# Optimization experiments

Hardware: AMD Instinct MI355X
Metric: run time of the kernel (lower is better)

The kernel has to match this reference:

```python
import jax, jax.numpy as jnp
import numpy as np

C = 32          # middle_channels
N_DOWN = 13     # layers 2..14, stride 2
DENSITY = 0.01  # nnz fraction of the 2048x2048 sparse matrix


def _conv(x, w):
    # centered SAME conv; inactive sites hold zeros so they contribute nothing,
    # matching MinkowskiConvolution's sum over existing neighbor coordinates.
    return jax.lax.conv_general_dilated(
        x, w, window_strides=(1, 1), padding='SAME',
        dimension_numbers=('NHWC', 'HWIO', 'NHWC'))


def _downsample_mask(mask):
    # ME stride-2 output coords = stride-quantized input coords -> OR over 2x2 block
    return jax.lax.reduce_window(mask, 0.0, jax.lax.max, (1, 2, 2), (1, 2, 2), 'SAME')


def _layer(x, mask, w, stride):
    y = _conv(x, w)
    if stride > 1:
        y = y[:, ::stride, ::stride, :]   # value at quantized coordinate u
        mask = _downsample_mask(mask)
    y = jax.nn.relu(y) * mask[..., None]  # ReLU on active sites, keep inactive = 0
    return y, mask


def _global_avg_pool(x, mask):
    cnt = jnp.maximum(jnp.sum(mask, axis=(1, 2)), 1.0)  # number of active coords
    return jnp.sum(x, axis=(1, 2)) / cnt[:, None]       # [B, C]


def setup_inputs() -> dict:
    key = jax.random.key(0)
    ks = jax.random.split(key, 8)
    H = W = 2048
    mask = (jax.random.uniform(ks[0], (1, H, W)) < DENSITY).astype(jnp.float32)
    x = jax.random.normal(ks[1], (1, H, W, 1), dtype=jnp.float32) * mask[..., None]
    # kaiming_normal fan_out (nonlinearity='relu') for conv kernels, bias=False in ME
    w1 = jax.random.normal(ks[2], (5, 5, 1, C), dtype=jnp.float32) * np.float32((2.0 / (5 * 5 * C)) ** 0.5)
    ws = jax.random.normal(ks[3], (N_DOWN, 3, 3, C, C), dtype=jnp.float32) * np.float32((2.0 / (3 * 3 * C)) ** 0.5)
    wm1 = jax.random.normal(ks[4], (C * 14, 256), dtype=jnp.float32) * np.float32((1.0 / (C * 14)) ** 0.5)
    bm1 = jnp.zeros((256,), jnp.float32)
    wm2 = jax.random.normal(ks[5], (256, 128), dtype=jnp.float32) * np.float32((1.0 / 256) ** 0.5)
    bm2 = jnp.zeros((128,), jnp.float32)
    return {'x': x, 'mask': mask, 'w1': w1, 'ws': ws,
            'wm1': wm1, 'bm1': bm1, 'wm2': wm2, 'bm2': bm2}


def reference(x, mask, w1, ws, wm1, bm1, wm2, bm2):
    y, m = _layer(x, mask, w1, stride=1)          # layer1: k=5, s=1
    pools = [_global_avg_pool(y, m)]
    for i in range(N_DOWN):                       # layers 2..14: k=3, s=2
        y, m = _layer(y, m, ws[i], stride=2)
        pools.append(_global_avg_pool(y, m))
    feat = jnp.concatenate(pools, axis=-1)        # [B, 32*14]
    h = jax.nn.relu(feat @ wm1 + bm1)
    return h @ wm2 + bm2                          # [B, 128]
```

## Files before the change

kernel.cpp:

```cpp
#include <hip/hip_runtime.h>

#define NLVL 14
#define NSHARD 16

struct ZeroArgs { unsigned long long zoff[13]; };

struct TailArgs {
    char* ws;
    const float* wm1; const float* bm1;
    const float* wm2; const float* bm2;
    float* out;
    unsigned long long idx8, idx9, idx10;
    unsigned long long nbr8, nbr9, nbr10;
    unsigned long long val7, val8, val9;
    int cap8, cap9, cap10;
};

__device__ __forceinline__ float fma4(float4 v, float4 w, float acc) {
    acc = fmaf(v.x, w.x, acc);
    acc = fmaf(v.y, w.y, acc);
    acc = fmaf(v.z, w.z, acc);
    return fmaf(v.w, w.w, acc);
}

__device__ __forceinline__ int cnt_load(const int* p) {
    return __hip_atomic_load(p, __ATOMIC_RELAXED, __HIP_MEMORY_SCOPE_AGENT);
}

__device__ __forceinline__ int block_scan_base(int mycnt, int* gcnt, int& myoff) {
    __shared__ int wsum[4];
    __shared__ int base;
    __syncthreads();
    int lane = threadIdx.x & 63, wid = threadIdx.x >> 6;
    int scan = mycnt;
    #pragma unroll
    for (int d = 1; d < 64; d <<= 1) {
        int tv = __shfl_up(scan, d, 64);
        if (lane >= d) scan += tv;
    }
    if (lane == 63) wsum[wid] = scan;
    __syncthreads();
    if (threadIdx.x == 0) {
        int tot = 0;
        #pragma unroll
        for (int i = 0; i < 4; i++) { int tv = wsum[i]; wsum[i] = tot; tot += tv; }
        base = tot ? atomicAdd(gcnt, tot) : 0;
    }
    __syncthreads();
    myoff = wsum[wid] + scan - mycnt;
    return base;
}

__device__ void compact0_tile(const float4* __restrict__ mask4, int* __restrict__ idxmap,
                              int* __restrict__ coords, int* __restrict__ cnt, int cap, int tile) {
    int t = threadIdx.x;
    int g0 = tile * 1024 + t;
    float4 m[4];
    #pragma unroll
    for (int j = 0; j < 4; j++) m[j] = mask4[g0 + j * 256];
    int pr[16];
    int mycnt = 0;
    #pragma unroll
    for (int j = 0; j < 4; j++) {
        pr[4 * j + 0] = m[j].x > 0.5f;
        pr[4 * j + 1] = m[j].y > 0.5f;
        pr[4 * j + 2] = m[j].z > 0.5f;
        pr[4 * j + 3] = m[j].w > 0.5f;
        mycnt += pr[4 * j] + pr[4 * j + 1] + pr[4 * j + 2] + pr[4 * j + 3];
    }
    int myoff;
    int base = block_scan_base(mycnt, cnt, myoff);
    int slot = base + myoff;
    #pragma unroll
    for (int j = 0; j < 4; j++) {
        int e0 = (g0 + j * 256) << 2;
        int wv[4];
        #pragma unroll
        for (int k = 0; k < 4; k++) {
            wv[k] = -1;
            if (pr[4 * j + k]) {
                int sl = slot++;
                if (sl < cap) { wv[k] = sl; coords[sl] = e0 + k; }
            }
        }
        *(int4*)(idxmap + e0) = make_int4(wv[0], wv[1], wv[2], wv[3]);
    }
}

__device__ void down_nbr(const int* __restrict__ idx_in, int HinB,
                         int* __restrict__ idx_out, int* __restrict__ nbr_out,
                         int* __restrict__ cnt_out, int HoutB, int cap_out,
                         int zofs, int bb) {
    int Hout = 1 << HoutB, Hin = 1 << HinB;
    int S = Hout * Hout;
    int S4 = (S + 3) >> 2;
    int o4 = bb * 256 + threadIdx.x;
    int e0 = o4 << 2;
    int jv[4][9];
    int pr[4] = {0, 0, 0, 0};
    #pragma unroll
    for (int k = 0; k < 4; k++)
        #pragma unroll
        for (int tap = 0; tap < 9; tap++) jv[k][tap] = -1;
    if (o4 < S4) {
        if (HoutB >= 2) {
            int r = e0 >> HoutB, c0 = e0 & (Hout - 1);
            int w[3][12];
            #pragma unroll
            for (int a = 0; a < 3; a++) {
                int rr = 2 * r + a - 1;
                bool rok = (unsigned)rr < (unsigned)Hin;
                const int* rowp = idx_in + ((size_t)(rok ? rr : 0) << HinB) + 2 * c0;
                int4 L = (rok && c0 > 0) ? *(const int4*)(rowp - 4) : make_int4(-1, -1, -1, -1);
                int4 M = rok ? *(const int4*)rowp : make_int4(-1, -1, -1, -1);
                int4 R = rok ? *(const int4*)(rowp + 4) : make_int4(-1, -1, -1, -1);
                w[a][0] = L.x; w[a][1] = L.y; w[a][2]  = L.z; w[a][3]  = L.w;
                w[a][4] = M.x; w[a][5] = M.y; w[a][6]  = M.z; w[a][7]  = M.w;
                w[a][8] = R.x; w[a][9] = R.y; w[a][10] = R.z; w[a][11] = R.w;
            }
            #pragma unroll
            for (int k = 0; k < 4; k++) {
                #pragma unroll
                for (int a = 0; a < 3; a++)
                    #pragma unroll
                    for (int b = 0; b < 3; b++)
                        jv[k][a * 3 + b] = w[a][2 * k + b + 3];
                pr[k] = ((jv[k][4] & jv[k][5] & jv[k][7] & jv[k][8]) >= 0);
            }
        } else {
            #pragma unroll
            for (int k = 0; k < 4; k++) {
                int p = e0 + k;
                if (p < S) {
                    int r = p >> HoutB, c = p & (Hout - 1);
                    #pragma unroll
                    for (int a = 0; a < 3; a++)
                        #pragma unroll
                        for (int b = 0; b < 3; b++) {
                            int rr = 2 * r + a - 1, cc = 2 * c + b - 1;
                            if ((unsigned)rr < (unsigned)Hin && (unsigned)cc < (unsigned)Hin)
                                jv[k][a * 3 + b] = idx_in[((size_t)rr << HinB) + cc];
                        }
                    pr[k] = ((jv[k][4] & jv[k][5] & jv[k][7] & jv[k][8]) >= 0);
                }
            }
        }
    }
    int mycnt = pr[0] + pr[1] + pr[2] + pr[3];
    int myoff;
    int base = block_scan_base(mycnt, cnt_out, myoff);
    int slot = base + myoff;
    int wv[4] = {-1, -1, -1, -1};
    #pragma unroll
    for (int k = 0; k < 4; k++) {
        if (pr[k]) {
            int sl = slot++;
            if (sl < cap_out) {
                wv[k] = sl;
                #pragma unroll
                for (int tap = 0; tap < 9; tap++) {
                    int j = jv[k][tap];
                    nbr_out[sl * 9 + tap] = (j < 0) ? zofs : (j << 7);
                }
            }
        }
    }
    if (o4 < S4) {
        if (S >= 4) *(int4*)(idx_out + e0) = make_int4(wv[0], wv[1], wv[2], wv[3]);
        else {
            #pragma unroll
            for (int k = 0; k < 4; k++) if (e0 + k < S) idx_out[e0 + k] = wv[k];
        }
    }
}

__device__ void down_small_wave(const int* __restrict__ idx_in, int HinB,
                                int* __restrict__ idx_out, int* __restrict__ nbr_out,
                                int* __restrict__ cnt_out, int HoutB, int cap_out,
                                int zofs) {
    int t = threadIdx.x;
    int Hout = 1 << HoutB, Hin = 1 << HinB, S = Hout * Hout;
    int p = t;
    int jv[9];
    int pr = 0;
    #pragma unroll
    for (int tap = 0; tap < 9; tap++) jv[tap] = -1;
    if (p < S) {
        int r = p >> HoutB, c = p & (Hout - 1);
        #pragma unroll
        for (int a = 0; a < 3; a++)
            #pragma unroll
            for (int b = 0; b < 3; b++) {
                int rr = 2 * r + a - 1, cc = 2 * c + b - 1;
                if ((unsigned)rr < (unsigned)Hin && (unsigned)cc < (unsigned)Hin)
                    jv[a * 3 + b] = idx_in[(rr << HinB) + cc];
            }
        pr = ((jv[4] & jv[5] & jv[7] & jv[8]) >= 0);
    }
    int scan = pr;
    #pragma unroll
    for (int d = 1; d < 64; d <<= 1) {
        int tv = __shfl_up(scan, d, 64);
        if (t >= d) scan += tv;
    }
    int myoff = scan - pr;
    int tot = __shfl(scan, 63, 64);
    if (p < S) {
        int wv = -1;
        if (pr && myoff < cap_out) {
            wv = myoff;
            #pragma unroll
            for (int tap = 0; tap < 9; tap++) {
                int j = jv[tap];
                nbr_out[myoff * 9 + tap] = (j < 0) ? zofs : (j << 7);
            }
        }
        idx_out[p] = wv;
    }
    if (t == 0 && tot) atomicAdd(cnt_out, tot);
}

__device__ void conv_small_1024(const char* __restrict__ vprevb,
                                const float* __restrict__ wlvl,
                                const int* __restrict__ nbr, int n,
                                float* __restrict__ vals, float* __restrict__ poolp) {
    __shared__ __align__(16) float s_in[576 * 32];
    int t = threadIdx.x;
    int ciq = t & 7, co = (t >> 3) & 31, sp = t >> 8;
    float4 wreg[9];
    #pragma unroll
    for (int tap = 0; tap < 9; tap++)
        wreg[tap] = *(const float4*)(wlvl + ((tap * 32 + co) << 5) + (ciq << 2));
    int items = n * 72;
    for (int i = t; i < items; i += 1024) {
        int row = i >> 3, q = i & 7;
        int jb = nbr[row];
        *(float4*)&s_in[(row << 5) + (q << 2)] =
            *(const float4*)(vprevb + jb + (q << 4));
    }
    __syncthreads();
    float ps = 0.f;
    #pragma unroll 1
    for (int gp = 0; gp < 16; gp++) {
        int g = gp * 4 + sp;
        if (g >= n) break;
        float a0 = 0.f;
        #pragma unroll
        for (int tap = 0; tap < 9; tap++) {
            float4 v = *(const float4*)&s_in[((g * 9 + tap) << 5) + (ciq << 2)];
            a0 = fma4(v, wreg[tap], a0);
        }
        a0 += __shfl_xor(a0, 1); a0 += __shfl_xor(a0, 2); a0 += __shfl_xor(a0, 4);
        if (ciq == 0) {
            float r0 = fmaxf(a0, 0.f);
            vals[((size_t)g << 5) + co] = r0;
            ps += r0;
        }
    }
    if (ciq == 0 && ps != 0.f) atomicAdd(&poolp[co], ps);
}

__device__ void conv_bs(const char* __restrict__ vprevb, const float* __restrict__ wlvl,
                        const int* __restrict__ nbr, int n,
                        float* __restrict__ vals, float* __restrict__ poolp,
                        int b0, int nbk, int shard) {
    __shared__ int s_j[144];
    __shared__ __align__(16) float s_in[144 * 32];
    int t = threadIdx.x;
    int ciq = t & 7, coh = (t >> 3) & 15, sp = t >> 7;
    float4 wreg[9][2];
    #pragma unroll
    for (int tap = 0; tap < 9; tap++) {
        wreg[tap][0] = *(const float4*)(wlvl + ((tap * 32 + coh) << 5) + (ciq << 2));
        wreg[tap][1] = *(const float4*)(wlvl + ((tap * 32 + coh + 16) << 5) + (ciq << 2));
    }
    float ps0 = 0.f, ps1 = 0.f;
    int ngr = (n + 15) >> 4;
    for (int grp = b0; grp < ngr; grp += nbk) {
        __syncthreads();
        if (t < 144) {
            int gi = grp * 144 + t;
            s_j[t] = (gi < n * 9) ? nbr[gi] : 0;
        }
        __syncthreads();
        #pragma unroll
        for (int i = t; i < 1152; i += 256) {
            int row = i >> 3, q = i & 7;
            *(float4*)&s_in[(row << 5) + (q << 2)] =
                *(const float4*)(vprevb + s_j[row] + (q << 4));
        }
        __syncthreads();
        #pragma unroll
        for (int gp = 0; gp < 8; gp++) {
            int g = gp * 2 + sp;
            int s = (grp << 4) + g;
            float4 v[9];
            #pragma unroll
            for (int tap = 0; tap < 9; tap++)
                v[tap] = *(const float4*)&s_in[((g * 9 + tap) << 5) + (ciq << 2)];
            float a0 = 0.f, a1 = 0.f;
            #pragma unroll
            for (int tap = 0; tap < 9; tap++) {
                a0 = fma4(v[tap], wreg[tap][0], a0);
                a1 = fma4(v[tap], wreg[tap][1], a1);
            }
            a0 += __shfl_xor(a0, 1); a0 += __shfl_xor(a0, 2); a0 += __shfl_xor(a0, 4);
            a1 += __shfl_xor(a1, 1); a1 += __shfl_xor(a1, 2); a1 += __shfl_xor(a1, 4);
            if (ciq == 0 && s < n) {
                float r0 = fmaxf(a0, 0.f), r1 = fmaxf(a1, 0.f);
                vals[((size_t)s << 5) + coh] = r0;
                vals[((size_t)s << 5) + coh + 16] = r1;
                ps0 += r0; ps1 += r1;
            }
        }
    }
    if (ciq == 0 && (ps0 != 0.f || ps1 != 0.f)) {
        atomicAdd(&poolp[shard * 448 + coh], ps0);
        atomicAdd(&poolp[shard * 448 + coh + 16], ps1);
    }
}

__device__ void conv0_bs(const float* __restrict__ x, const float* __restrict__ w1,
                         const int* __restrict__ coords0, int n,
                         float* __restrict__ vals0, float* __restrict__ poolp,
                         int b0, int nbk, int shard) {
    __shared__ float lw[800];
    __shared__ float lx[8][28];
    __shared__ float red[256];
    int t = threadIdx.x;
    for (int i = t; i < 800; i += 256) lw[i] = w1[i];
    int sl = t >> 5, ch = t & 31;
    float psum = 0.f;
    int ngr = (n + 7) >> 3;
    for (int grp = b0; grp < ngr; grp += nbk) {
        __syncthreads();
        if (t < 200) {
            int slot = t / 25, tap = t - slot * 25;
            int s = (grp << 3) + slot;
            float v = 0.f;
            if (s < n) {
                int p = coords0[s];
                int r = p >> 11, c = p & 2047;
                int a = tap / 5, b = tap - a * 5;
                int rr = r + a - 2, cc = c + b - 2;
                if ((unsigned)rr < 2048u && (unsigned)cc < 2048u)
                    v = x[(rr << 11) + cc];
            }
            lx[slot][tap] = v;
        }
        __syncthreads();
        int s = (grp << 3) + sl;
        float acc = 0.f;
        #pragma unroll
        for (int tap = 0; tap < 25; tap++)
            acc = fmaf(lx[sl][tap], lw[tap * 32 + ch], acc);
        if (s < n) {
            float r0 = fmaxf(acc, 0.f);
            vals0[((size_t)s << 5) + ch] = r0;
            psum += r0;
        }
    }
    __syncthreads();
    red[t] = psum;
    __syncthreads();
    if (t < 32) {
        float tot = 0.f;
        #pragma unroll
        for (int q = 0; q < 8; q++) tot += red[t + 32 * q];
        if (tot != 0.f) atomicAdd(&poolp[shard * 448 + t], tot);
    }
}

__global__ __launch_bounds__(256) void k_f0(
    const float4* __restrict__ mask4, int* __restrict__ idxmap,
    int* __restrict__ coords, int* __restrict__ cnt, int cap,
    const float* __restrict__ w, float* __restrict__ wt,
    char* __restrict__ wsbase, ZeroArgs za) {
    if (blockIdx.x == 1492) {
        for (int i = threadIdx.x; i < 13 * 32; i += 256)
            *(float*)(wsbase + za.zoff[i >> 5] + ((i & 31) << 2)) = 0.f;
        return;
    }
    if (blockIdx.x >= 1024) {
        int t = (int)(blockIdx.x - 1024) * 256 + threadIdx.x;
        if (t < 13 * 9 * 32 * 32) {
            int ci = t & 31, co = (t >> 5) & 31, tp = t >> 10;
            wt[(tp << 10) + (co << 5) + ci] = w[(tp << 10) + (ci << 5) + co];
        }
        return;
    }
    compact0_tile(mask4, idxmap, coords, cnt, cap, blockIdx.x);
}

__global__ __launch_bounds__(256) void k_f1(
    const int* __restrict__ idx0, int* __restrict__ idx1, int* __restrict__ nbr1,
    int* __restrict__ cnt1, int cap1, int zofs1,
    const float* __restrict__ x, const float* __restrict__ w1,
    const int* __restrict__ coords0, const int* __restrict__ cnt0, int cap0,
    float* __restrict__ vals0, float* __restrict__ poolp,
    const float* __restrict__ wm1, const float* __restrict__ wm2, float* __restrict__ dummy) {
    if (blockIdx.x < 1024) {
        down_nbr(idx0, 11, idx1, nbr1, cnt1, 10, cap1, zofs1, blockIdx.x);
        return;
    }
    if (blockIdx.x >= 5120) {
        int t = (int)(blockIdx.x - 5120) * 256 + threadIdx.x;
        const float4* a = (const float4*)wm1;
        const float4* b = (const float4*)wm2;
        float acc = 0.f;
        for (int i = t; i < 28672; i += 6144) { float4 v = a[i]; acc += v.x + v.y + v.z + v.w; }
        for (int i = t; i < 8192; i += 6144)  { float4 v = b[i]; acc += v.x + v.y + v.z + v.w; }
        if (acc == 1234.56789f) dummy[0] = acc;
        return;
    }
    int n = *cnt0; if (n > cap0) n = cap0;
    conv0_bs(x, w1, coords0, n, vals0, poolp, blockIdx.x - 1024, 4096, blockIdx.x & (NSHARD - 1));
}

__global__ __launch_bounds__(256) void k_flevel(
    int downB,
    const int* __restrict__ idx_in, int HinB,
    int* __restrict__ idx_out, int* __restrict__ nbr_out, int* __restrict__ cnt_out,
    int HoutB, int cap_out, int zofs,
    const char* __restrict__ vprevb, const float* __restrict__ wlvl,
    const int* __restrict__ nbr_c, const int* __restrict__ cnt_c, int cap_c,
    float* __restrict__ vals_c, float* __restrict__ poolp) {
    if ((int)blockIdx.x < downB) {
        down_nbr(idx_in, HinB, idx_out, nbr_out, cnt_out, HoutB, cap_out, zofs, blockIdx.x);
        return;
    }
    int n = *cnt_c; if (n > cap_c) n = cap_c;
    conv_bs(vprevb, wlvl, nbr_c, n, vals_c, poolp,
            blockIdx.x - downB, gridDim.x - downB, blockIdx.x & (NSHARD - 1));
}

__global__ __launch_bounds__(1024) void k_tail3(TailArgs a) {
    char* ws = a.ws;
    int* cnt = (int*)ws;
    float* poolsh = (float*)(ws + 256);
    float* wt = (float*)(ws + 32768);
    int t = threadIdx.x;

    if (t < 64)
        down_small_wave((const int*)(ws + a.idx8), 3, (int*)(ws + a.idx9),
                        (int*)(ws + a.nbr9), cnt + 9, 2, a.cap9, a.cap8 * 128);
    __syncthreads();
    {
        int n8 = cnt_load(cnt + 8); if (n8 > a.cap8) n8 = a.cap8;
        conv_small_1024((const char*)(ws + a.val7), wt + (size_t)7 * 9216,
                        (const int*)(ws + a.nbr8), n8,
                        (float*)(ws + a.val8), poolsh + 8 * 32);
    }
    __syncthreads();
    if (t < 64)
        down_small_wave((const int*)(ws + a.idx9), 2, (int*)(ws + a.idx10),
                        (int*)(ws + a.nbr10), cnt + 10, 1, a.cap10, a.cap9 * 128);
    __syncthreads();
    {
        int n9 = cnt_load(cnt + 9); if (n9 > a.cap9) n9 = a.cap9;
        conv_small_1024((const char*)(ws + a.val8), wt + (size_t)8 * 9216,
                        (const int*)(ws + a.nbr9), n9,
                        (float*)(ws + a.val9), poolsh + 9 * 32);
    }
    __syncthreads();

    const char* vals9b = (const char*)(ws + a.val9);
    const int* nbr10 = (const int*)(ws + a.nbr10);
    const int* idx10 = (const int*)(ws + a.idx10);
    __shared__ __align__(16) float v10[128];
    __shared__ float v11[32], v12[32], v13[32];
    __shared__ float feat[448], h[256], part[1024];
    __shared__ int s_i10[4], s_n10;
    int ciq = t & 7, co = (t >> 3) & 31, s = t >> 8;
    int ciq16 = ciq << 4;
    if (t == 0) s_n10 = cnt_load(cnt + 10);
    if (t < 4) s_i10[t] = idx10[t];
    __syncthreads();
    int n10 = s_n10; if (n10 > 4) n10 = 4;
    {
        const float* wl = wt + (size_t)9 * 9216;
        float4 wreg[9];
        #pragma unroll
        for (int tap = 0; tap < 9; tap++)
            wreg[tap] = *(const float4*)(wl + ((tap * 32 + co) << 5) + (ciq << 2));
        bool live = s < n10;
        int sb = live ? s : 0;
        float a0 = 0.f;
        #pragma unroll
        for (int tap = 0; tap < 9; tap++)
            a0 = fma4(*(const float4*)(vals9b + nbr10[sb * 9 + tap] + ciq16), wreg[tap], a0);
        a0 += __shfl_xor(a0, 1); a0 += __shfl_xor(a0, 2); a0 += __shfl_xor(a0, 4);
        if (ciq == 0 && live) v10[s * 32 + co] = fmaxf(a0, 0.f);
    }
    __syncthreads();
    int i10[4] = {s_i10[0], s_i10[1], s_i10[2], s_i10[3]};
    int nbr11[9];
    #pragma unroll
    for (int tap = 0; tap < 9; tap++) {
        int aa = tap / 3, bb = tap - aa * 3;
        int rr = aa - 1, cc = bb - 1;
        nbr11[tap] = ((unsigned)rr < 2u && (unsigned)cc < 2u) ? i10[rr * 2 + cc] : -1;
    }
    int n11 = ((nbr11[4] & nbr11[5] & nbr11[7] & nbr11[8]) >= 0) ? 1 : 0;
    if (s == 0) {
        const float* wl = wt + (size_t)10 * 9216;
        float a0 = 0.f;
        #pragma unroll
        for (int tap = 0; tap < 9; tap++) {
            int j = nbr11[tap];
            if (j >= 0) {
                float4 wv = *(const float4*)(wl + ((tap * 32 + co) << 5) + (ciq << 2));
                a0 = fma4(*(const float4*)(&v10[(j << 5) + (ciq << 2)]), wv, a0);
            }
        }
        a0 += __shfl_xor(a0, 1); a0 += __shfl_xor(a0, 2); a0 += __shfl_xor(a0, 4);
        if (ciq == 0) v11[co] = n11 ? fmaxf(a0, 0.f) : 0.f;
    }
    __syncthreads();
    if (s == 0) {
        const float* wl = wt + (size_t)11 * 9216;
        float4 wv = *(const float4*)(wl + ((4 * 32 + co) << 5) + (ciq << 2));
        float a0 = n11 ? fma4(*(const float4*)(&v11[ciq << 2]), wv, 0.f) : 0.f;
        a0 += __shfl_xor(a0, 1); a0 += __shfl_xor(a0, 2); a0 += __shfl_xor(a0, 4);
        if (ciq == 0) v12[co] = n11 ? fmaxf(a0, 0.f) : 0.f;
    }
    __syncthreads();
    if (s == 0) {
        const float* wl = wt + (size_t)12 * 9216;
        float4 wv = *(const float4*)(wl + ((4 * 32 + co) << 5) + (ciq << 2));
        float a0 = n11 ? fma4(*(const float4*)(&v12[ciq << 2]), wv, 0.f) : 0.f;
        a0 += __shfl_xor(a0, 1); a0 += __shfl_xor(a0, 2); a0 += __shfl_xor(a0, 4);
        if (ciq == 0) v13[co] = n11 ? fmaxf(a0, 0.f) : 0.f;
    }
    __syncthreads();
    if (t < 320) {
        float sum = 0.f;
        #pragma unroll
        for (int sh = 0; sh < NSHARD; sh++) sum += poolsh[sh * 448 + t];
        float c = (float)cnt_load(cnt + (t >> 5)); if (c < 1.f) c = 1.f;
        feat[t] = sum / c;
    }
    if (t < 32) {
        float s10 = 0.f;
        for (int q = 0; q < n10; q++) s10 += v10[q * 32 + t];
        float c10 = (float)n10; if (c10 < 1.f) c10 = 1.f;
        feat[320 + t] = s10 / c10;
        feat[352 + t] = n11 ? v11[t] : 0.f;
        feat[384 + t] = n11 ? v12[t] : 0.f;
        feat[416 + t] = n11 ? v13[t] : 0.f;
    }
    __syncthreads();
    {
        int j = t & 255, chunk = t >> 8;
        float acc = (chunk == 0) ? a.bm1[j] : 0.f;
        int k0 = chunk * 112;
        #pragma unroll 8
        for (int k = k0; k < k0 + 112; k++) acc = fmaf(feat[k], a.wm1[k * 256 + j], acc);
        part[t] = acc;
    }
    __syncthreads();
    if (t < 256)
        h[t] = fmaxf(part[t] + part[t + 256] + part[t + 512] + part[t + 768], 0.f);
    __syncthreads();
    {
        int j2 = t & 127, c2 = t >> 7;
        float a2 = (c2 == 0) ? a.bm2[j2] : 0.f;
        int kk0 = c2 * 32;
        #pragma unroll 8
        for (int k = kk0; k < kk0 + 32; k++) a2 = fmaf(h[k], a.wm2[k * 128 + j2], a2);
        part[t] = a2;
    }
    __syncthreads();
    if (t < 128) {
        float sum = 0.f;
        #pragma unroll
        for (int c = 0; c < 8; c++) sum += part[t + 128 * c];
        a.out[t] = sum;
    }
}

extern "C" void kernel_launch(void* const* d_in, const int* in_sizes, int n_in,
                              void* d_out, int out_size, void* d_ws, size_t ws_size,
                              hipStream_t stream) {
    const float* x    = (const float*)d_in[0];
    const float* mask = (const float*)d_in[1];
    const float* w1   = (const float*)d_in[2];
    const float* wsrc = (const float*)d_in[3];
    const float* wm1  = (const float*)d_in[4];
    const float* bm1  = (const float*)d_in[5];
    const float* wm2  = (const float*)d_in[6];
    const float* bm2  = (const float*)d_in[7];
    float* out = (float*)d_out;
    char* ws = (char*)d_ws;

    static const int Hb[NLVL]   = {11, 10, 9, 8, 7, 6, 5, 4, 3, 2, 1, 0, 0, 0};
    static const int caps[NLVL] = {45056, 43008, 43008, 34816, 16384, 4096,
                                   1024, 256, 64, 16, 4, 1, 1, 1};

    size_t pool_off = 256;
    size_t wt_off = 32768;
    size_t off = wt_off + (size_t)13 * 9 * 1024 * 4;
    off = (off + 255) & ~(size_t)255;
    size_t coord0_off = off; off += (size_t)caps[0] * 4; off = (off + 255) & ~(size_t)255;
    size_t idx_off[NLVL], nbr_off[NLVL], val_off[NLVL];
    for (int l = 0; l < NLVL; l++) {
        size_t S = (size_t)(1 << Hb[l]) * (1 << Hb[l]);
        size_t sb = S * 4; if (sb < 16) sb = 16;
        idx_off[l] = off; off += sb; off = (off + 255) & ~(size_t)255;
        if (l >= 1) { nbr_off[l] = off; off += (size_t)caps[l] * 36; off = (off + 255) & ~(size_t)255; }
        else nbr_off[l] = 0;
        val_off[l] = off; off += (size_t)(caps[l] + 1) * 128; off = (off + 255) & ~(size_t)255;
    }

    int* cnt = (int*)ws;
    float* poolsh = (float*)(ws + pool_off);
    float* dummy = (float*)(ws + 128);
    float* wt = (float*)(ws + wt_off);

    ZeroArgs za;
    for (int l = 0; l < 13; l++) za.zoff[l] = val_off[l] + (size_t)caps[l] * 128;

    hipMemsetAsync(ws, 0, 32768, stream);

    k_f0<<<1493, 256, 0, stream>>>(
        (const float4*)mask, (int*)(ws + idx_off[0]), (int*)(ws + coord0_off),
        cnt, caps[0], wsrc, wt, ws, za);

    k_f1<<<5144, 256, 0, stream>>>(
        (const int*)(ws + idx_off[0]), (int*)(ws + idx_off[1]), (int*)(ws + nbr_off[1]),
        cnt + 1, caps[1], caps[0] * 128,
        x, w1, (const int*)(ws + coord0_off), cnt, caps[0],
        (float*)(ws + val_off[0]), poolsh, wm1, wm2, dummy);

    for (int i = 2; i <= 8; i++) {
        int lc = i - 1;
        int Hout = 1 << Hb[i];
        int S4 = (Hout * Hout + 3) >> 2;
        int downB = (S4 + 255) >> 8; if (downB < 1) downB = 1;
        int convB = (caps[lc] + 15) >> 4;
        if (convB > 768) convB = 768;
        k_flevel<<<downB + convB, 256, 0, stream>>>(
            downB,
            (const int*)(ws + idx_off[i - 1]), Hb[i - 1],
            (int*)(ws + idx_off[i]), (int*)(ws + nbr_off[i]), cnt + i, Hb[i], caps[i],
            caps[i - 1] * 128,
            (const char*)(ws + val_off[lc - 1]), wt + (size_t)(lc - 1) * 9216,
            (const int*)(ws + nbr_off[lc]), cnt + lc, caps[lc],
            (float*)(ws + val_off[lc]), poolsh + lc * 32);
    }

    TailArgs ta;
    ta.ws = ws;
    ta.wm1 = wm1; ta.bm1 = bm1; ta.wm2 = wm2; ta.bm2 = bm2;
    ta.out = out;
    ta.idx8 = idx_off[8];  ta.idx9 = idx_off[9];  ta.idx10 = idx_off[10];
    ta.nbr8 = nbr_off[8];  ta.nbr9 = nbr_off[9];  ta.nbr10 = nbr_off[10];
    ta.val7 = val_off[7];  ta.val8 = val_off[8];  ta.val9 = val_off[9];
    ta.cap8 = caps[8]; ta.cap9 = caps[9]; ta.cap10 = caps[10];
    k_tail3<<<1, 1024, 0, stream>>>(ta);
}
```

Before: 257.8 us.

## Double-buffer conv_bs gather with async global-to-LDS loads and index prefetch

The neighbour-feature gather in conv_bs now uses global_load_lds (16-byte direct-to-LDS loads) into a double-buffered shared tile. The next group's tile is issued before the current group is computed, and the neighbour indices for the group after that are preloaded into a register. The goal is to hide gather latency behind the FMA work and drop the register staging of the old load loop. In exchange it doubles LDS use, which may lower occupancy, and it depends on the barrier at the top of the loop to wait for the async LDS writes before they are read.

```diff
diff --git a/kernel.cpp b/kernel.cpp
--- a/kernel.cpp
+++ b/kernel.cpp
@@ -26,6 +26,10 @@
 __device__ __forceinline__ int cnt_load(const int* p) {
     return __hip_atomic_load(p, __ATOMIC_RELAXED, __HIP_MEMORY_SCOPE_AGENT);
 }
+
+#define GLDS16(gsrc, ldst) __builtin_amdgcn_global_load_lds( \
+    (const __attribute__((address_space(1))) void*)(gsrc),   \
+    (__attribute__((address_space(3))) void*)(ldst), 16, 0, 0)
 
 __device__ __forceinline__ int block_scan_base(int mycnt, int* gcnt, int& myoff) {
     __shared__ int wsum[4];
@@ -264,10 +268,11 @@
                         const int* __restrict__ nbr, int n,
                         float* __restrict__ vals, float* __restrict__ poolp,
                         int b0, int nbk, int shard) {
-    __shared__ int s_j[144];
-    __shared__ __align__(16) float s_in[144 * 32];
+    __shared__ int s_j[2][144];
+    __shared__ __align__(16) float s_in[2][144 * 32];
     int t = threadIdx.x;
     int ciq = t & 7, coh = (t >> 3) & 15, sp = t >> 7;
+    int wid = t >> 6, lane = t & 63;
     float4 wreg[9][2];
     #pragma unroll
     for (int tap = 0; tap < 9; tap++) {
@@ -276,20 +281,58 @@
     }
     float ps0 = 0.f, ps1 = 0.f;
     int ngr = (n + 15) >> 4;
+    int n9 = n * 9;
+
+    int jreg = 0;
+    if (t < 144) {
+        int gi = b0 * 144 + t;
+        jreg = (b0 < ngr && gi < n9) ? nbr[gi] : 0;
+        s_j[0][t] = jreg;
+    }
+    __syncthreads();
+    if (b0 < ngr) {
+        const int* sj = s_j[0];
+        #pragma unroll
+        for (int inst = 0; inst < 5; inst++) {
+            int ii = wid + inst * 4;
+            if (ii < 18) {
+                int chunk = (ii << 6) + lane;
+                int row = chunk >> 3, q = chunk & 7;
+                GLDS16(vprevb + sj[row] + (q << 4), &s_in[0][ii << 8]);
+            }
+        }
+    }
+    if (t < 144) {
+        int g1 = b0 + nbk;
+        int gi = g1 * 144 + t;
+        jreg = (g1 < ngr && gi < n9) ? nbr[gi] : 0;
+    }
+
+    int cur = 0;
     for (int grp = b0; grp < ngr; grp += nbk) {
         __syncthreads();
+        bool hasnext = (grp + nbk) < ngr;
+        if (t < 144) s_j[cur ^ 1][t] = jreg;
+        __syncthreads();
+        if (hasnext) {
+            const int* sj = s_j[cur ^ 1];
+            float* dst = s_in[cur ^ 1];
+            #pragma unroll
+            for (int inst = 0; inst < 5; inst++) {
+                int ii = wid + inst * 4;
+                if (ii < 18) {
+                    int chunk = (ii << 6) + lane;
+                    int row = chunk >> 3, q = chunk & 7;
+                    GLDS16(vprevb + sj[row] + (q << 4), &dst[ii << 8]);
+                }
+            }
+        }
         if (t < 144) {
-            int gi = grp * 144 + t;
-            s_j[t] = (gi < n * 9) ? nbr[gi] : 0;
-        }
-        __syncthreads();
-        #pragma unroll
-        for (int i = t; i < 1152; i += 256) {
-            int row = i >> 3, q = i & 7;
-            *(float4*)&s_in[(row << 5) + (q << 2)] =
-                *(const float4*)(vprevb + s_j[row] + (q << 4));
-        }
-        __syncthreads();
+            int g2 = grp + 2 * nbk;
+            int gi = g2 * 144 + t;
+            jreg = (g2 < ngr && gi < n9) ? nbr[gi] : 0;
+        }
+        const float* sb = s_in[cur];
         #pragma unroll
         for (int gp = 0; gp < 8; gp++) {
             int g = gp * 2 + sp;
@@ -297,7 +340,7 @@
             float4 v[9];
             #pragma unroll
             for (int tap = 0; tap < 9; tap++)
-                v[tap] = *(const float4*)&s_in[((g * 9 + tap) << 5) + (ciq << 2)];
+                v[tap] = *(const float4*)&sb[((g * 9 + tap) << 5) + (ciq << 2)];
             float a0 = 0.f, a1 = 0.f;
             #pragma unroll
             for (int tap = 0; tap < 9; tap++) {
@@ -313,6 +356,7 @@
                 ps0 += r0; ps1 += r1;
             }
         }
+        cur ^= 1;
     }
     if (ciq == 0 && (ps0 != 0.f || ps1 != 0.f)) {
         atomicAdd(&poolp[shard * 448 + coh], ps0);
```

New measurement: 244.1 us, median of 2. 1.06x faster.
